# Kernel tuning notes

Hardware: AMD Instinct MI355X
Metric: run time of the kernel (lower is better)

Reference implementation:

```python
import jax, jax.numpy as jnp
import numpy as np
import math

EMBED_DIM = 512
NUM_CLASSES = 100000
BATCH = 512
MARGIN = 0.5
SCALE = 64.0
EASY_MARGIN = False
COS_M = math.cos(MARGIN)
SIN_M = math.sin(MARGIN)
TH = math.cos(math.pi - MARGIN)
MM = math.sin(math.pi - MARGIN) * MARGIN


def setup_inputs() -> dict:
    key = jax.random.key(0)
    k1, k2, k3 = jax.random.split(key, 3)
    inp = jax.random.normal(k1, (BATCH, EMBED_DIM), dtype=jnp.float32)
    # xavier-uniform init for weight [num_classes, embedding_dim]
    limit = math.sqrt(6.0 / (NUM_CLASSES + EMBED_DIM))
    weight = jax.random.uniform(k2, (NUM_CLASSES, EMBED_DIM), dtype=jnp.float32,
                                minval=-limit, maxval=limit)
    target = jax.random.randint(k3, (BATCH,), 0, NUM_CLASSES, dtype=jnp.int64)
    return {"input": inp, "weight": weight, "target": target}


def _l2_normalize(x, axis, eps=1e-12):
    # matches F.normalize(p=2): x / max(||x||, eps)
    n = jnp.sqrt(jnp.sum(x * x, axis=axis, keepdims=True))
    return x / jnp.maximum(n, eps)


def reference(input, weight, target):
    x = _l2_normalize(input, axis=1)                      # [B, D]
    w = _l2_normalize(weight, axis=1)                     # [C, D]
    cosine = jnp.einsum('bd,cd->bc', x, w)                # [B, C]
    # margin only affects the target logit; compute it per-row (same math as
    # the full-matrix where + one_hot blend in the original).
    cos_t = jnp.take_along_axis(cosine, target[:, None].astype(jnp.int32), axis=1)[:, 0]  # [B]
    sin_t = jnp.sqrt(jnp.clip(1.0 - cos_t * cos_t, 0.0, None))
    phi_t = cos_t * COS_M - sin_t * SIN_M
    if EASY_MARGIN:
        phi_t = jnp.where(cos_t > 0, phi_t, cos_t)
    else:
        phi_t = jnp.where(cos_t > TH, phi_t, cos_t - MM)
    # cross-entropy with scaled logits: logsumexp over modified logits - target logit
    # modified logits differ from `cosine*SCALE` only at the target column.
    rows = jnp.arange(cosine.shape[0])
    logits = cosine.at[rows, target.astype(jnp.int32)].set(phi_t) * SCALE  # [B, C]
    lse = jax.scipy.special.logsumexp(logits, axis=1)     # [B]
    loss = jnp.mean(lse - SCALE * phi_t)
    return loss
```

## Files before the change

kernel.cpp:

```cpp
#include <hip/hip_runtime.h>
#include <math.h>


#define NB 512
#define ND 512
#define NC 100000
#define BK 32
#define NCHUNK 16
#define CT 64
#define FSCALE 64.0f
#define C_COS_M 0.8775825618903728f
#define C_SIN_M 0.479425538604203f
#define C_TH  (-0.8775825618903728f)
#define C_MM  0.2397127693021015f

typedef __bf16 bf16x8 __attribute__((ext_vector_type(8)));
typedef __bf16 bf16x4 __attribute__((ext_vector_type(4)));
typedef float  f32x4  __attribute__((ext_vector_type(4)));
typedef __attribute__((address_space(1))) unsigned int GU;
typedef __attribute__((address_space(3))) unsigned int LU;

__global__ void pack_x_kernel(const float* __restrict__ x, __bf16* __restrict__ xp) {
  const int b = blockIdx.x;
  const int t = threadIdx.x;
  float4 v = reinterpret_cast<const float4*>(x + (size_t)b * ND)[t];
  float ss = v.x*v.x + v.y*v.y + v.z*v.z + v.w*v.w;
  #pragma unroll
  for (int m = 1; m < 64; m <<= 1) ss += __shfl_xor(ss, m);
  __shared__ float sred[2];
  if ((t & 63) == 0) sred[t >> 6] = ss;
  __syncthreads();
  const float rn = rsqrtf(fmaxf(sred[0] + sred[1], 1e-24f));
  bf16x4 o;
  o[0] = (__bf16)(v.x * rn); o[1] = (__bf16)(v.y * rn);
  o[2] = (__bf16)(v.z * rn); o[3] = (__bf16)(v.w * rn);
  const int k = 4 * t;
  __bf16* dst = xp + ((size_t)(k >> 5) * NB + b) * BK + (k & 31);
  *reinterpret_cast<bf16x4*>(dst) = o;
}

__global__ void cosphi_kernel(const float* __restrict__ x, const float* __restrict__ w,
                              const int* __restrict__ tgt,
                              float* __restrict__ cos_t, float* __restrict__ phi_t) {
  const int b = blockIdx.x;
  const int lane = threadIdx.x;
  const int t = tgt[b];
  const float4* xr = reinterpret_cast<const float4*>(x + (size_t)b * ND);
  const float4* wr = reinterpret_cast<const float4*>(w + (size_t)t * ND);
  float dp = 0.f, xs = 0.f, ws = 0.f;
  #pragma unroll
  for (int j = 0; j < 2; ++j) {
    float4 xv = xr[lane * 2 + j];
    float4 wv = wr[lane * 2 + j];
    dp += xv.x*wv.x + xv.y*wv.y + xv.z*wv.z + xv.w*wv.w;
    xs += xv.x*xv.x + xv.y*xv.y + xv.z*xv.z + xv.w*xv.w;
    ws += wv.x*wv.x + wv.y*wv.y + wv.z*wv.z + wv.w*wv.w;
  }
  #pragma unroll
  for (int m = 1; m < 64; m <<= 1) {
    dp += __shfl_xor(dp, m);
    xs += __shfl_xor(xs, m);
    ws += __shfl_xor(ws, m);
  }
  if (lane == 0) {
    float c = dp * rsqrtf(fmaxf(xs, 1e-24f)) * rsqrtf(fmaxf(ws, 1e-24f));
    c = fminf(fmaxf(c, -1.f), 1.f);
    float s = sqrtf(fmaxf(1.f - c * c, 0.f));
    float phi = c * C_COS_M - s * C_SIN_M;
    phi = (c > C_TH) ? phi : (c - C_MM);
    cos_t[b] = c;
    phi_t[b] = phi;
  }
}

__global__ __launch_bounds__(512) void gemm_lse_kernel(
    const __bf16* __restrict__ xp, const float* __restrict__ w,
    float* __restrict__ gsum) {
  __shared__ __align__(16) __bf16 As[NB * BK];
  __shared__ __align__(16) __bf16 Bs[CT * BK];
  __shared__ float wss[CT];

  const int tid  = threadIdx.x;
  const int wv   = tid >> 6;
  const int lane = tid & 63;
  const int bc   = blockIdx.x * CT;

  const int wr = tid >> 3;
  const int wp = tid & 7;
  const long long wrow = (long long)min(bc + wr, NC - 1);
  const float4* wsrc = reinterpret_cast<const float4*>(w + wrow * (long long)ND);

  float wsq = 0.f;
  f32x4 acc[4][4] = {};

  const int m_w = wv * 64;
  const int qa  = (lane >> 4) * 8;
  const int ra  = lane & 15;

  for (int i = 0; i < NCHUNK; ++i) {
    __syncthreads();
    {
      const char* g = reinterpret_cast<const char*>(xp)
                      + (size_t)i * (NB * BK * 2) + wv * 1024 + lane * 16;
      char* l = reinterpret_cast<char*>(As) + wv * 1024;
      #pragma unroll
      for (int j = 0; j < 4; ++j) {
        __builtin_amdgcn_global_load_lds((GU*)(g + j * 8192), (LU*)(l + j * 8192),
                                         16, 0, 0);
      }
    }
    {
      float4 v = wsrc[i * 8 + wp];
      wsq += v.x*v.x + v.y*v.y + v.z*v.z + v.w*v.w;
      bf16x4 pk;
      pk[0] = (__bf16)v.x; pk[1] = (__bf16)v.y;
      pk[2] = (__bf16)v.z; pk[3] = (__bf16)v.w;
      *reinterpret_cast<bf16x4*>(Bs + wr * BK + wp * 4) = pk;
    }
    __syncthreads();

    bf16x8 af[4], bfr[4];
    #pragma unroll
    for (int rt = 0; rt < 4; ++rt)
      af[rt] = *reinterpret_cast<const bf16x8*>(As + (m_w + rt * 16 + ra) * BK + qa);
    #pragma unroll
    for (int ct = 0; ct < 4; ++ct)
      bfr[ct] = *reinterpret_cast<const bf16x8*>(Bs + (ct * 16 + ra) * BK + qa);
    #pragma unroll
    for (int rt = 0; rt < 4; ++rt)
      #pragma unroll
      for (int ct = 0; ct < 4; ++ct)
        acc[rt][ct] = __builtin_amdgcn_mfma_f32_16x16x32_bf16(af[rt], bfr[ct],
                                                              acc[rt][ct], 0, 0, 0);
  }

  wsq += __shfl_xor(wsq, 1);
  wsq += __shfl_xor(wsq, 2);
  wsq += __shfl_xor(wsq, 4);
  if (wp == 0) wss[wr] = wsq;
  __syncthreads();

  const int col_l = lane & 15;
  const int quad  = lane >> 4;
  float rnw[4];
  int   vmask[4];
  #pragma unroll
  for (int ct = 0; ct < 4; ++ct) {
    rnw[ct]   = rsqrtf(fmaxf(wss[ct * 16 + col_l], 1e-24f));
    vmask[ct] = (bc + ct * 16 + col_l) < NC;
  }
  #pragma unroll
  for (int rt = 0; rt < 4; ++rt) {
    #pragma unroll
    for (int r = 0; r < 4; ++r) {
      float es = 0.f;
      #pragma unroll
      for (int ct = 0; ct < 4; ++ct) {
        float cosv = acc[rt][ct][r] * rnw[ct];
        float e = __expf(fmaf(FSCALE, cosv, -FSCALE));
        es += vmask[ct] ? e : 0.f;
      }
      es += __shfl_xor(es, 1);
      es += __shfl_xor(es, 2);
      es += __shfl_xor(es, 4);
      es += __shfl_xor(es, 8);
      if (col_l == 0) {
        atomicAdd(&gsum[m_w + rt * 16 + quad * 4 + r], es);
      }
    }
  }
}

__global__ void finalize_kernel(const float* __restrict__ gsum,
                                const float* __restrict__ cos_t,
                                const float* __restrict__ phi_t,
                                float* __restrict__ out) {
  const int b = threadIdx.x;
  const float c = cos_t[b];
  const float p = phi_t[b];
  float corr = gsum[b] - __expf(fmaf(FSCALE, c, -FSCALE))
                       + __expf(fmaf(FSCALE, p, -FSCALE));
  corr = fmaxf(corr, 1e-38f);
  float lb = FSCALE + logf(corr) - FSCALE * p;
  #pragma unroll
  for (int m = 1; m < 64; m <<= 1) lb += __shfl_xor(lb, m);
  __shared__ float pr[8];
  if ((b & 63) == 0) pr[b >> 6] = lb;
  __syncthreads();
  if (b == 0) {
    float tot = 0.f;
    #pragma unroll
    for (int j = 0; j < 8; ++j) tot += pr[j];
    out[0] = tot * (1.0f / NB);
  }
}

extern "C" void kernel_launch(void* const* d_in, const int* in_sizes, int n_in,
                              void* d_out, int out_size, void* d_ws, size_t ws_size,
                              hipStream_t stream) {
  const float* x  = (const float*)d_in[0];
  const float* w  = (const float*)d_in[1];
  const int* tgt  = (const int*)d_in[2];
  float* out      = (float*)d_out;

  __bf16* xp   = (__bf16*)d_ws;
  float* gsum  = (float*)((char*)d_ws + (size_t)NB * ND * 2);
  float* cos_t = gsum + NB;
  float* phi_t = cos_t + NB;

  hipMemsetAsync(gsum, 0, NB * sizeof(float), stream);
  pack_x_kernel<<<NB, 128, 0, stream>>>(x, xp);
  cosphi_kernel<<<NB, 64, 0, stream>>>(x, w, tgt, cos_t, phi_t);
  const int nblk = (NC + CT - 1) / CT;
  gemm_lse_kernel<<<nblk, 512, 0, stream>>>(xp, w, gsum);
  finalize_kernel<<<1, 512, 0, stream>>>(gsum, cos_t, phi_t, out);
}
```

Before: 431.5 us.

## Double-buffer LDS tiles to overlap next-chunk loads with MFMA compute

Splits the A (packed x) and B (converted weight) shared-memory tiles into two buffers and prefetches chunk c+1 while MFMAs run on chunk c. This drops one barrier per iteration and aims to hide global-load latency behind compute. Launch bounds also ask for four blocks per SM (`__launch_bounds__(512, 4)`), which may force register limits. LDS use roughly doubles to about 72KB, which could reduce occupancy and conflict with that request.

After: 498.3 us. +15.5%, slower.

```diff
diff --git a/kernel.cpp b/kernel.cpp
--- a/kernel.cpp
+++ b/kernel.cpp
@@ -73,11 +73,11 @@
   }
 }
 
-__global__ __launch_bounds__(512) void gemm_lse_kernel(
+__global__ __launch_bounds__(512, 4) void gemm_lse_kernel(
     const __bf16* __restrict__ xp, const float* __restrict__ w,
     float* __restrict__ gsum) {
-  __shared__ __align__(16) __bf16 As[NB * BK];
-  __shared__ __align__(16) __bf16 Bs[CT * BK];
+  __shared__ __align__(16) __bf16 As[2][NB * BK];
+  __shared__ __align__(16) __bf16 Bs[2][CT * BK];
   __shared__ float wss[CT];
 
   const int tid  = threadIdx.x;
@@ -97,41 +97,59 @@
   const int qa  = (lane >> 4) * 8;
   const int ra  = lane & 15;
 
-  for (int i = 0; i < NCHUNK; ++i) {
-    __syncthreads();
-    {
+  {
+    float4 v = wsrc[wp];
+    const char* g = reinterpret_cast<const char*>(xp) + wv * 1024 + lane * 16;
+    char* l = reinterpret_cast<char*>(&As[0][0]) + wv * 1024;
+    #pragma unroll
+    for (int j = 0; j < 4; ++j)
+      __builtin_amdgcn_global_load_lds((GU*)(g + j * 8192), (LU*)(l + j * 8192),
+                                       16, 0, 0);
+    wsq += v.x*v.x + v.y*v.y + v.z*v.z + v.w*v.w;
+    bf16x4 pk;
+    pk[0] = (__bf16)v.x; pk[1] = (__bf16)v.y;
+    pk[2] = (__bf16)v.z; pk[3] = (__bf16)v.w;
+    *reinterpret_cast<bf16x4*>(&Bs[0][wr * BK + wp * 4]) = pk;
+  }
+  __syncthreads();
+
+  for (int c = 0; c < NCHUNK; ++c) {
+    const int cur = c & 1;
+    const bool more = (c + 1 < NCHUNK);
+    float4 vn;
+    if (more) {
+      vn = wsrc[(c + 1) * 8 + wp];
       const char* g = reinterpret_cast<const char*>(xp)
-                      + (size_t)i * (NB * BK * 2) + wv * 1024 + lane * 16;
-      char* l = reinterpret_cast<char*>(As) + wv * 1024;
+                      + (size_t)(c + 1) * (NB * BK * 2) + wv * 1024 + lane * 16;
+      char* l = reinterpret_cast<char*>(&As[cur ^ 1][0]) + wv * 1024;
       #pragma unroll
-      for (int j = 0; j < 4; ++j) {
+      for (int j = 0; j < 4; ++j)
         __builtin_amdgcn_global_load_lds((GU*)(g + j * 8192), (LU*)(l + j * 8192),
                                          16, 0, 0);
-      }
     }
-    {
-      float4 v = wsrc[i * 8 + wp];
-      wsq += v.x*v.x + v.y*v.y + v.z*v.z + v.w*v.w;
-      bf16x4 pk;
-      pk[0] = (__bf16)v.x; pk[1] = (__bf16)v.y;
-      pk[2] = (__bf16)v.z; pk[3] = (__bf16)v.w;
-      *reinterpret_cast<bf16x4*>(Bs + wr * BK + wp * 4) = pk;
-    }
-    __syncthreads();
 
     bf16x8 af[4], bfr[4];
     #pragma unroll
     for (int rt = 0; rt < 4; ++rt)
-      af[rt] = *reinterpret_cast<const bf16x8*>(As + (m_w + rt * 16 + ra) * BK + qa);
+      af[rt] = *reinterpret_cast<const bf16x8*>(&As[cur][(m_w + rt * 16 + ra) * BK + qa]);
     #pragma unroll
     for (int ct = 0; ct < 4; ++ct)
-      bfr[ct] = *reinterpret_cast<const bf16x8*>(Bs + (ct * 16 + ra) * BK + qa);
+      bfr[ct] = *reinterpret_cast<const bf16x8*>(&Bs[cur][(ct * 16 + ra) * BK + qa]);
     #pragma unroll
     for (int rt = 0; rt < 4; ++rt)
       #pragma unroll
       for (int ct = 0; ct < 4; ++ct)
         acc[rt][ct] = __builtin_amdgcn_mfma_f32_16x16x32_bf16(af[rt], bfr[ct],
                                                               acc[rt][ct], 0, 0, 0);
+
+    if (more) {
+      wsq += vn.x*vn.x + vn.y*vn.y + vn.z*vn.z + vn.w*vn.w;
+      bf16x4 pk;
+      pk[0] = (__bf16)vn.x; pk[1] = (__bf16)vn.y;
+      pk[2] = (__bf16)vn.z; pk[3] = (__bf16)vn.w;
+      *reinterpret_cast<bf16x4*>(&Bs[cur ^ 1][wr * BK + wp * 4]) = pk;
+    }
+    __syncthreads();
   }
 
   wsq += __shfl_xor(wsq, 1);
```

## Double-buffer X tiles, preload full W tile, swizzle LDS, use 1024-thread blocks

Applied to the files above, without the earlier changes.

The GEMM+LSE kernel now loads and converts its whole 64-row weight tile into LDS once, before the K loop, instead of once per chunk. It double-buffers the X chunk with async global-to-LDS loads, so the next chunk is prefetched while MFMAs run, and it needs only one barrier per chunk. An XOR swizzle is applied to both LDS layouts, including the packed X in the workspace, to cut bank conflicts. Blocks grow to 1024 threads with 32 rows per wave. In exchange the kernel uses more LDS per block, which may limit occupancy, and the whole W load is exposed up front.

Result: slower. 449.8 us (+4.2%).

```diff
diff --git a/kernel.cpp b/kernel.cpp
--- a/kernel.cpp
+++ b/kernel.cpp
@@ -14,6 +14,8 @@
 #define C_TH  (-0.8775825618903728f)
 #define C_MM  0.2397127693021015f
 
+#define SWZ(b) ((b) ^ (((b) >> 3) & 48))
+
 typedef __bf16 bf16x8 __attribute__((ext_vector_type(8)));
 typedef __bf16 bf16x4 __attribute__((ext_vector_type(4)));
 typedef float  f32x4  __attribute__((ext_vector_type(4)));
@@ -35,7 +37,9 @@
   o[0] = (__bf16)(v.x * rn); o[1] = (__bf16)(v.y * rn);
   o[2] = (__bf16)(v.z * rn); o[3] = (__bf16)(v.w * rn);
   const int k = 4 * t;
-  __bf16* dst = xp + ((size_t)(k >> 5) * NB + b) * BK + (k & 31);
+  const int chunk = k >> 5;
+  const int lb = b * 64 + (k & 31) * 2;
+  char* dst = (char*)xp + (size_t)chunk * (NB * BK * 2) + SWZ(lb);
   *reinterpret_cast<bf16x4*>(dst) = o;
 }
 
@@ -73,71 +77,92 @@
   }
 }
 
-__global__ __launch_bounds__(512) void gemm_lse_kernel(
+__global__ __launch_bounds__(1024) void gemm_lse_kernel(
     const __bf16* __restrict__ xp, const float* __restrict__ w,
     float* __restrict__ gsum) {
-  __shared__ __align__(16) __bf16 As[NB * BK];
-  __shared__ __align__(16) __bf16 Bs[CT * BK];
-  __shared__ float wss[CT];
+  __shared__ __align__(16) char As[2 * NB * BK * 2];
+  __shared__ __align__(16) char Bs[NCHUNK * CT * BK * 2];
 
   const int tid  = threadIdx.x;
   const int wv   = tid >> 6;
   const int lane = tid & 63;
   const int bc   = blockIdx.x * CT;
 
-  const int wr = tid >> 3;
-  const int wp = tid & 7;
-  const long long wrow = (long long)min(bc + wr, NC - 1);
+  {
+    const char* g = (const char*)xp + wv * 1024 + lane * 16;
+    char* l = As + wv * 1024;
+    __builtin_amdgcn_global_load_lds((GU*)g,           (LU*)l,           16, 0, 0);
+    __builtin_amdgcn_global_load_lds((GU*)(g + 16384), (LU*)(l + 16384), 16, 0, 0);
+  }
+
+  const int r  = tid >> 4;
+  const int wp = tid & 15;
+  const long long wrow = (long long)min(bc + r, NC - 1);
   const float4* wsrc = reinterpret_cast<const float4*>(w + wrow * (long long)ND);
-
   float wsq = 0.f;
-  f32x4 acc[4][4] = {};
-
-  const int m_w = wv * 64;
-  const int qa  = (lane >> 4) * 8;
+  #pragma unroll
+  for (int i = 0; i < 8; ++i) {
+    float4 v = wsrc[i * 16 + wp];
+    wsq += v.x*v.x + v.y*v.y + v.z*v.z + v.w*v.w;
+    bf16x4 pk;
+    pk[0] = (__bf16)v.x; pk[1] = (__bf16)v.y;
+    pk[2] = (__bf16)v.z; pk[3] = (__bf16)v.w;
+    const int k4 = (i * 16 + wp) * 4;
+    const int chunk = k4 >> 5;
+    const int lb = r * 64 + (k4 & 31) * 2;
+    *reinterpret_cast<bf16x4*>(Bs + chunk * (CT * BK * 2) + SWZ(lb)) = pk;
+  }
+  __syncthreads();
+
+  const int m_w = wv * 32;
   const int ra  = lane & 15;
-
-  for (int i = 0; i < NCHUNK; ++i) {
-    __syncthreads();
-    {
-      const char* g = reinterpret_cast<const char*>(xp)
-                      + (size_t)i * (NB * BK * 2) + wv * 1024 + lane * 16;
-      char* l = reinterpret_cast<char*>(As) + wv * 1024;
-      #pragma unroll
-      for (int j = 0; j < 4; ++j) {
-        __builtin_amdgcn_global_load_lds((GU*)(g + j * 8192), (LU*)(l + j * 8192),
-                                         16, 0, 0);
-      }
+  const int qb  = (lane >> 4) * 16;
+  int aoff[2], boff[4];
+  #pragma unroll
+  for (int rt = 0; rt < 2; ++rt) {
+    const int lb = (m_w + rt * 16 + ra) * 64 + qb;
+    aoff[rt] = SWZ(lb);
+  }
+  #pragma unroll
+  for (int ct = 0; ct < 4; ++ct) {
+    const int lb = (ct * 16 + ra) * 64 + qb;
+    boff[ct] = SWZ(lb);
+  }
+
+  f32x4 acc[2][4] = {};
+
+  for (int c = 0; c < NCHUNK; ++c) {
+    const int cur = c & 1;
+    if (c + 1 < NCHUNK) {
+      const char* g = (const char*)xp + (size_t)(c + 1) * (NB * BK * 2)
+                      + wv * 1024 + lane * 16;
+      char* l = As + (cur ^ 1) * (NB * BK * 2) + wv * 1024;
+      __builtin_amdgcn_global_load_lds((GU*)g,           (LU*)l,           16, 0, 0);
+      __builtin_amdgcn_global_load_lds((GU*)(g + 16384), (LU*)(l + 16384), 16, 0, 0);
     }
-    {
-      float4 v = wsrc[i * 8 + wp];
-      wsq += v.x*v.x + v.y*v.y + v.z*v.z + v.w*v.w;
-      bf16x4 pk;
-      pk[0] = (__bf16)v.x; pk[1] = (__bf16)v.y;
-      pk[2] = (__bf16)v.z; pk[3] = (__bf16)v.w;
-      *reinterpret_cast<bf16x4*>(Bs + wr * BK + wp * 4) = pk;
-    }
-    __syncthreads();
-
-    bf16x8 af[4], bfr[4];
-    #pragma unroll
-    for (int rt = 0; rt < 4; ++rt)
-      af[rt] = *reinterpret_cast<const bf16x8*>(As + (m_w + rt * 16 + ra) * BK + qa);
+
+    bf16x8 af[2], bfr[4];
+    #pragma unroll
+    for (int rt = 0; rt < 2; ++rt)
+      af[rt] = *reinterpret_cast<const bf16x8*>(As + cur * (NB * BK * 2) + aoff[rt]);
     #pragma unroll
     for (int ct = 0; ct < 4; ++ct)
-      bfr[ct] = *reinterpret_cast<const bf16x8*>(Bs + (ct * 16 + ra) * BK + qa);
-    #pragma unroll
-    for (int rt = 0; rt < 4; ++rt)
+      bfr[ct] = *reinterpret_cast<const bf16x8*>(Bs + c * (CT * BK * 2) + boff[ct]);
+    #pragma unroll
+    for (int rt = 0; rt < 2; ++rt)
       #pragma unroll
       for (int ct = 0; ct < 4; ++ct)
         acc[rt][ct] = __builtin_amdgcn_mfma_f32_16x16x32_bf16(af[rt], bfr[ct],
                                                               acc[rt][ct], 0, 0, 0);
+    __syncthreads();
   }
 
   wsq += __shfl_xor(wsq, 1);
   wsq += __shfl_xor(wsq, 2);
   wsq += __shfl_xor(wsq, 4);
-  if (wp == 0) wss[wr] = wsq;
+  wsq += __shfl_xor(wsq, 8);
+  float* wss = reinterpret_cast<float*>(As);
+  if (wp == 0) wss[r] = wsq;
   __syncthreads();
 
   const int col_l = lane & 15;
@@ -150,13 +175,13 @@
     vmask[ct] = (bc + ct * 16 + col_l) < NC;
   }
   #pragma unroll
-  for (int rt = 0; rt < 4; ++rt) {
-    #pragma unroll
-    for (int r = 0; r < 4; ++r) {
+  for (int rt = 0; rt < 2; ++rt) {
+    #pragma unroll
+    for (int rg = 0; rg < 4; ++rg) {
       float es = 0.f;
       #pragma unroll
       for (int ct = 0; ct < 4; ++ct) {
-        float cosv = acc[rt][ct][r] * rnw[ct];
+        float cosv = acc[rt][ct][rg] * rnw[ct];
         float e = __expf(fmaf(FSCALE, cosv, -FSCALE));
         es += vmask[ct] ? e : 0.f;
       }
@@ -165,7 +190,7 @@
       es += __shfl_xor(es, 4);
       es += __shfl_xor(es, 8);
       if (col_l == 0) {
-        atomicAdd(&gsum[m_w + rt * 16 + quad * 4 + r], es);
+        atomicAdd(&gsum[m_w + rt * 16 + quad * 4 + rg], es);
       }
     }
   }
@@ -212,6 +237,6 @@
   pack_x_kernel<<<NB, 128, 0, stream>>>(x, xp);
   cosphi_kernel<<<NB, 64, 0, stream>>>(x, w, tgt, cos_t, phi_t);
   const int nblk = (NC + CT - 1) / CT;
-  gemm_lse_kernel<<<nblk, 512, 0, stream>>>(xp, w, gsum);
+  gemm_lse_kernel<<<nblk, 1024, 0, stream>>>(xp, w, gsum);
   finalize_kernel<<<1, 512, 0, stream>>>(gsum, cos_t, phi_t, out);
 }
```

## Double-buffer GEMM tiles with async LDS loads, swizzle LDS, replicate LSE accumulators

Applied to the files above, without the earlier changes.

The GEMM loop now double-buffers both the packed x tile and the raw fp32 weight tile in LDS using global_load_lds, so the next chunk's loads overlap the current MFMAs and one barrier per iteration is dropped. LDS layouts are XOR-swizzled to avoid bank conflicts. The weight norms are computed from the LDS fragments in registers. Row-sum atomics are spread over 64 replica buffers that the finalize kernel reduces, cutting atomic contention. In exchange it uses more LDS and adds a launch-bounds occupancy hint.

Result: faster. 381.9 us (-11.5%).

```diff
diff --git a/kernel.cpp b/kernel.cpp
--- a/kernel.cpp
+++ b/kernel.cpp
@@ -8,11 +8,15 @@
 #define BK 32
 #define NCHUNK 16
 #define CT 64
+#define REP 64
 #define FSCALE 64.0f
 #define C_COS_M 0.8775825618903728f
 #define C_SIN_M 0.479425538604203f
 #define C_TH  (-0.8775825618903728f)
 #define C_MM  0.2397127693021015f
+
+#define SWZA(b) ((b) ^ (((b) >> 3) & 48))
+#define SWZW(b) ((b) ^ (((b) >> 3) & 112))
 
 typedef __bf16 bf16x8 __attribute__((ext_vector_type(8)));
 typedef __bf16 bf16x4 __attribute__((ext_vector_type(4)));
@@ -35,7 +39,9 @@
   o[0] = (__bf16)(v.x * rn); o[1] = (__bf16)(v.y * rn);
   o[2] = (__bf16)(v.z * rn); o[3] = (__bf16)(v.w * rn);
   const int k = 4 * t;
-  __bf16* dst = xp + ((size_t)(k >> 5) * NB + b) * BK + (k & 31);
+  const int chunk = k >> 5;
+  const int lb = b * 64 + (k & 31) * 2;
+  char* dst = (char*)xp + (size_t)chunk * (NB * BK * 2) + SWZA(lb);
   *reinterpret_cast<bf16x4*>(dst) = o;
 }
 
@@ -73,90 +79,107 @@
   }
 }
 
-__global__ __launch_bounds__(512) void gemm_lse_kernel(
+__global__ __launch_bounds__(512, 4) void gemm_lse_kernel(
     const __bf16* __restrict__ xp, const float* __restrict__ w,
     float* __restrict__ gsum) {
-  __shared__ __align__(16) __bf16 As[NB * BK];
-  __shared__ __align__(16) __bf16 Bs[CT * BK];
-  __shared__ float wss[CT];
+  __shared__ __align__(16) char As[2 * NB * BK * 2];
+  __shared__ __align__(16) char Ws[2 * CT * BK * 4];
 
   const int tid  = threadIdx.x;
   const int wv   = tid >> 6;
   const int lane = tid & 63;
   const int bc   = blockIdx.x * CT;
 
-  const int wr = tid >> 3;
-  const int wp = tid & 7;
-  const long long wrow = (long long)min(bc + wr, NC - 1);
-  const float4* wsrc = reinterpret_cast<const float4*>(w + wrow * (long long)ND);
-
-  float wsq = 0.f;
+  const int p_w   = wv * 1024 + lane * 16;
+  const int lbw   = SWZW(p_w);
+  const int wrow  = min(bc + (lbw >> 7), NC - 1);
+  const char* wg  = (const char*)w + (size_t)wrow * (ND * 4) + (lbw & 127);
+
+  const char* ag = (const char*)xp + wv * 1024 + lane * 16;
+
+  {
+    char* la = As + wv * 1024;
+    #pragma unroll
+    for (int j = 0; j < 4; ++j)
+      __builtin_amdgcn_global_load_lds((const GU*)(ag + j * 8192),
+                                       (LU*)(la + j * 8192), 16, 0, 0);
+    __builtin_amdgcn_global_load_lds((const GU*)wg, (LU*)(Ws + wv * 1024), 16, 0, 0);
+  }
+
+  const int m_w  = wv * 64;
+  const int ra   = lane & 15;
+  const int quad = lane >> 4;
+  int aoff[4], woff[4];
+  #pragma unroll
+  for (int rt = 0; rt < 4; ++rt)
+    aoff[rt] = SWZA((m_w + rt * 16 + ra) * 64 + quad * 16);
+  #pragma unroll
+  for (int ct = 0; ct < 4; ++ct)
+    woff[ct] = SWZW((ct * 16 + ra) * 128 + quad * 32);
+
   f32x4 acc[4][4] = {};
-
-  const int m_w = wv * 64;
-  const int qa  = (lane >> 4) * 8;
-  const int ra  = lane & 15;
-
-  for (int i = 0; i < NCHUNK; ++i) {
-    __syncthreads();
-    {
-      const char* g = reinterpret_cast<const char*>(xp)
-                      + (size_t)i * (NB * BK * 2) + wv * 1024 + lane * 16;
-      char* l = reinterpret_cast<char*>(As) + wv * 1024;
+  float wsq[4] = {0.f, 0.f, 0.f, 0.f};
+
+  __syncthreads();
+
+  for (int c = 0; c < NCHUNK; ++c) {
+    const int cur = c & 1;
+    if (c + 1 < NCHUNK) {
+      const char* a1 = ag + (size_t)(c + 1) * (NB * BK * 2);
+      char* la = As + (cur ^ 1) * (NB * BK * 2) + wv * 1024;
       #pragma unroll
-      for (int j = 0; j < 4; ++j) {
-        __builtin_amdgcn_global_load_lds((GU*)(g + j * 8192), (LU*)(l + j * 8192),
-                                         16, 0, 0);
-      }
+      for (int j = 0; j < 4; ++j)
+        __builtin_amdgcn_global_load_lds((const GU*)(a1 + j * 8192),
+                                         (LU*)(la + j * 8192), 16, 0, 0);
+      __builtin_amdgcn_global_load_lds((const GU*)(wg + (size_t)(c + 1) * 128),
+                                       (LU*)(Ws + (cur ^ 1) * 8192 + wv * 1024),
+                                       16, 0, 0);
     }
-    {
-      float4 v = wsrc[i * 8 + wp];
-      wsq += v.x*v.x + v.y*v.y + v.z*v.z + v.w*v.w;
-      bf16x4 pk;
-      pk[0] = (__bf16)v.x; pk[1] = (__bf16)v.y;
-      pk[2] = (__bf16)v.z; pk[3] = (__bf16)v.w;
-      *reinterpret_cast<bf16x4*>(Bs + wr * BK + wp * 4) = pk;
+
+    const char* asb = As + cur * (NB * BK * 2);
+    const char* wsb = Ws + cur * 8192;
+    bf16x8 af[4];
+    #pragma unroll
+    for (int rt = 0; rt < 4; ++rt)
+      af[rt] = *reinterpret_cast<const bf16x8*>(asb + aoff[rt]);
+    #pragma unroll
+    for (int ct = 0; ct < 4; ++ct) {
+      float4 w0 = *reinterpret_cast<const float4*>(wsb + woff[ct]);
+      float4 w1 = *reinterpret_cast<const float4*>(wsb + woff[ct] + 16);
+      wsq[ct] += w0.x*w0.x + w0.y*w0.y + w0.z*w0.z + w0.w*w0.w
+               + w1.x*w1.x + w1.y*w1.y + w1.z*w1.z + w1.w*w1.w;
+      bf16x8 bfr;
+      bfr[0] = (__bf16)w0.x; bfr[1] = (__bf16)w0.y;
+      bfr[2] = (__bf16)w0.z; bfr[3] = (__bf16)w0.w;
+      bfr[4] = (__bf16)w1.x; bfr[5] = (__bf16)w1.y;
+      bfr[6] = (__bf16)w1.z; bfr[7] = (__bf16)w1.w;
+      #pragma unroll
+      for (int rt = 0; rt < 4; ++rt)
+        acc[rt][ct] = __builtin_amdgcn_mfma_f32_16x16x32_bf16(af[rt], bfr,
+                                                              acc[rt][ct], 0, 0, 0);
     }
     __syncthreads();
-
-    bf16x8 af[4], bfr[4];
-    #pragma unroll
-    for (int rt = 0; rt < 4; ++rt)
-      af[rt] = *reinterpret_cast<const bf16x8*>(As + (m_w + rt * 16 + ra) * BK + qa);
-    #pragma unroll
-    for (int ct = 0; ct < 4; ++ct)
-      bfr[ct] = *reinterpret_cast<const bf16x8*>(Bs + (ct * 16 + ra) * BK + qa);
-    #pragma unroll
-    for (int rt = 0; rt < 4; ++rt)
-      #pragma unroll
-      for (int ct = 0; ct < 4; ++ct)
-        acc[rt][ct] = __builtin_amdgcn_mfma_f32_16x16x32_bf16(af[rt], bfr[ct],
-                                                              acc[rt][ct], 0, 0, 0);
-  }
-
-  wsq += __shfl_xor(wsq, 1);
-  wsq += __shfl_xor(wsq, 2);
-  wsq += __shfl_xor(wsq, 4);
-  if (wp == 0) wss[wr] = wsq;
-  __syncthreads();
-
-  const int col_l = lane & 15;
-  const int quad  = lane >> 4;
+  }
+
   float rnw[4];
   int   vmask[4];
   #pragma unroll
   for (int ct = 0; ct < 4; ++ct) {
-    rnw[ct]   = rsqrtf(fmaxf(wss[ct * 16 + col_l], 1e-24f));
-    vmask[ct] = (bc + ct * 16 + col_l) < NC;
-  }
+    wsq[ct] += __shfl_xor(wsq[ct], 16);
+    wsq[ct] += __shfl_xor(wsq[ct], 32);
+    rnw[ct]   = rsqrtf(fmaxf(wsq[ct], 1e-24f));
+    vmask[ct] = (bc + ct * 16 + ra) < NC;
+  }
+
+  float* gs = gsum + (size_t)(blockIdx.x & (REP - 1)) * NB;
   #pragma unroll
   for (int rt = 0; rt < 4; ++rt) {
     #pragma unroll
-    for (int r = 0; r < 4; ++r) {
+    for (int rg = 0; rg < 4; ++rg) {
       float es = 0.f;
       #pragma unroll
       for (int ct = 0; ct < 4; ++ct) {
-        float cosv = acc[rt][ct][r] * rnw[ct];
+        float cosv = acc[rt][ct][rg] * rnw[ct];
         float e = __expf(fmaf(FSCALE, cosv, -FSCALE));
         es += vmask[ct] ? e : 0.f;
       }
@@ -164,8 +187,8 @@
       es += __shfl_xor(es, 2);
       es += __shfl_xor(es, 4);
       es += __shfl_xor(es, 8);
-      if (col_l == 0) {
-        atomicAdd(&gsum[m_w + rt * 16 + quad * 4 + r], es);
+      if (ra == 0) {
+        atomicAdd(&gs[m_w + rt * 16 + quad * 4 + rg], es);
       }
     }
   }
@@ -176,10 +199,13 @@
                                 const float* __restrict__ phi_t,
                                 float* __restrict__ out) {
   const int b = threadIdx.x;
+  float s = 0.f;
+  #pragma unroll 8
+  for (int r = 0; r < REP; ++r) s += gsum[r * NB + b];
   const float c = cos_t[b];
   const float p = phi_t[b];
-  float corr = gsum[b] - __expf(fmaf(FSCALE, c, -FSCALE))
-                       + __expf(fmaf(FSCALE, p, -FSCALE));
+  float corr = s - __expf(fmaf(FSCALE, c, -FSCALE))
+                 + __expf(fmaf(FSCALE, p, -FSCALE));
   corr = fmaxf(corr, 1e-38f);
   float lb = FSCALE + logf(corr) - FSCALE * p;
   #pragma unroll
@@ -205,10 +231,10 @@
 
   __bf16* xp   = (__bf16*)d_ws;
   float* gsum  = (float*)((char*)d_ws + (size_t)NB * ND * 2);
-  float* cos_t = gsum + NB;
+  float* cos_t = gsum + (size_t)REP * NB;
   float* phi_t = cos_t + NB;
 
-  hipMemsetAsync(gsum, 0, NB * sizeof(float), stream);
+  hipMemsetAsync(gsum, 0, (size_t)REP * NB * sizeof(float), stream);
   pack_x_kernel<<<NB, 128, 0, stream>>>(x, xp);
   cosphi_kernel<<<NB, 64, 0, stream>>>(x, w, tgt, cos_t, phi_t);
   const int nblk = (NC + CT - 1) / CT;
```
